# Optimization experiments

Measured on AMD Instinct MI355X. Metric: run time of the kernel, lower is better.

## Reference

```python
import jax, jax.numpy as jnp
import numpy as np

N = 100000   # nodes
H = 96       # hidden_dim
A = 32       # attn_dim
De = 16      # edge_embeddings_dim
E = 500000   # edges per edge type
NEG_SLOPE = 0.01  # torch F.leaky_relu default


def setup_inputs() -> dict:
    key = jax.random.key(0)
    ks = jax.random.split(key, 24)
    nrm = lambda k, shape, s=1.0: jax.random.normal(k, shape, dtype=jnp.float32) * s
    idx = lambda k: jax.random.randint(k, (E,), 0, N, dtype=jnp.int32)
    Din = 2 * H + De
    return {
        'h': nrm(ks[0], (N, H)),
        'src0': idx(ks[1]), 'dst0': idx(ks[2]),
        'src1': idx(ks[3]), 'dst1': idx(ks[4]),
        'src2': idx(ks[5]), 'dst2': idx(ks[6]),
        'Wm0': nrm(ks[7], (Din, H), Din ** -0.5), 'bm0': jnp.zeros((H,), jnp.float32), 'ef0': nrm(ks[8], (De,)),
        'Wm1': nrm(ks[9], (Din, H), Din ** -0.5), 'bm1': jnp.zeros((H,), jnp.float32), 'ef1': nrm(ks[10], (De,)),
        'Wm2': nrm(ks[11], (Din, H), Din ** -0.5), 'bm2': jnp.zeros((H,), jnp.float32), 'ef2': nrm(ks[12], (De,)),
        'Wn0': nrm(ks[13], (H, A), H ** -0.5), 'Wa0': nrm(ks[14], (2 * A, 1), (2 * A) ** -0.5),
        'Wn1': nrm(ks[15], (H, A), H ** -0.5), 'Wa1': nrm(ks[16], (2 * A, 1), (2 * A) ** -0.5),
        'Wu': nrm(ks[17], (4 * H, H), (4 * H) ** -0.5), 'bu': jnp.zeros((H,), jnp.float32),
    }


def _leaky(x):
    return jnp.where(x > 0, x, NEG_SLOPE * x)


def _edge_msg(h, src, dst, Wm, bm, ef):
    # cat(src_h, dst_h, edge_feature) -> Linear  (dropout p=0, eval mode)
    x = jnp.concatenate([h[src], h[dst], jnp.broadcast_to(ef, (src.shape[0], ef.shape[0]))], axis=-1)
    return x @ Wm + bm  # [E, H]


def _mean_agg(m, dst):
    # fn.mean('m','msg'): per-destination mean over incoming edges
    s = jax.ops.segment_sum(m, dst, num_segments=N)
    c = jax.ops.segment_sum(jnp.ones((m.shape[0],), m.dtype), dst, num_segments=N)
    return s / jnp.maximum(c, 1.0)[:, None]


def _attn_agg(scores, m, dst):
    # per-destination softmax over mailbox (variable-size), then weighted sum
    smax = jax.ops.segment_max(scores, dst, num_segments=N)
    ex = jnp.exp(scores - smax[dst])
    den = jax.ops.segment_sum(ex, dst, num_segments=N)
    num = jax.ops.segment_sum(ex[:, None] * m, dst, num_segments=N)
    return num / jnp.maximum(den, 1e-9)[:, None]


def reference(h, src0, dst0, src1, dst1, src2, dst2,
              Wm0, bm0, ef0, Wm1, bm1, ef1, Wm2, bm2, ef2,
              Wn0, Wa0, Wn1, Wa1, Wu, bu):
    # edge type 0: intra_diff (attention), type 1: inter_diff (attention), type 2: intra_lt (mean)
    m0 = _edge_msg(h, src0, dst0, Wm0, bm0, ef0)
    m1 = _edge_msg(h, src1, dst1, Wm1, bm1, ef1)
    m2 = _edge_msg(h, src2, dst2, Wm2, bm2, ef2)

    z0 = h @ Wn0  # [N, A]
    s0 = _leaky(jnp.concatenate([z0[src0], z0[dst0]], axis=-1) @ Wa0)[:, 0]  # [E]
    z1 = h @ Wn1
    s1 = _leaky(jnp.concatenate([z1[src1], z1[dst1]], axis=-1) @ Wa1)[:, 0]

    msg0 = _attn_agg(s0, m0, dst0)   # [N, H]
    msg1 = _attn_agg(s1, m1, dst1)
    msg2 = _mean_agg(m2, dst2)

    # cross_reducer='stack' then concat over edge-type dim -> [N, 3H]
    mcat = jnp.concatenate([msg0, msg1, msg2], axis=-1)
    # cell node update: Linear(cat(h, m)) + ReLU
    return jax.nn.relu(jnp.concatenate([h, mcat], axis=-1) @ Wu + bu)
```

## Files before the change

kernel.cpp:

```cpp
#include <hip/hip_runtime.h>
#include <hip/hip_bf16.h>
#include <cstdint>

#define NN 100000
#define HH 96
#define AD 32
#define DE 16
#define EE 500000
#define NEG 0.01f

#define GSH 10
#define GSZ 1024
#define KB 98
#define CH 4096
#define BPT 123

typedef __bf16 bf16x8 __attribute__((ext_vector_type(8)));
typedef float  f32x4  __attribute__((ext_vector_type(4)));

__device__ __forceinline__ unsigned short f2b(float x) {
    union { float f; unsigned int u; } v; v.f = x;
    unsigned int r = v.u + 0x7fffu + ((v.u >> 16) & 1u);
    return (unsigned short)(r >> 16);
}
__device__ __forceinline__ float b2f(unsigned short h) {
    union { unsigned int u; float f; } v; v.u = ((unsigned int)h) << 16;
    return v.f;
}

__global__ void prep_kernel(const float* Wm0, const float* bm0, const float* ef0,
                            const float* Wm1, const float* bm1, const float* ef1,
                            const float* Wm2, const float* bm2, const float* ef2,
                            const float* Wn0, const float* Wa0,
                            const float* Wn1, const float* Wa1,
                            const float* Wu,
                            float* cvec, float* wvec,
                            unsigned short* BfN, unsigned short* BfU) {
    const float* Wm[3] = {Wm0, Wm1, Wm2};
    const float* bm[3] = {bm0, bm1, bm2};
    const float* ef[3] = {ef0, ef1, ef2};
    const int total = 288 + 384 + 55296 + 36864;
    for (int i = blockIdx.x * blockDim.x + threadIdx.x; i < total;
         i += gridDim.x * blockDim.x) {
        if (i < 288) {
            int t = i / 96, j = i % 96;
            float s = bm[t][j];
            for (int k = 0; k < DE; ++k) s += ef[t][k] * Wm[t][(2 * HH + k) * HH + j];
            cvec[i] = s;
        } else if (i < 288 + 384) {
            int ii = i - 288;
            int kind = ii / 96, k = ii % 96;
            const float* Wn = (kind < 2) ? Wn0 : Wn1;
            const float* Wa = (kind < 2) ? Wa0 : Wa1;
            int off = (kind & 1) ? AD : 0;
            float s = 0.f;
            for (int a = 0; a < AD; ++a) s += Wn[k * AD + a] * Wa[off + a];
            wvec[ii] = s;
        } else if (i < 288 + 384 + 55296) {
            int ii = i - 672;
            int sec = ii / 9216; int rem = ii % 9216;
            int ksc = rem / 512; int lj = rem % 512;
            int ks = ksc / 6, c = ksc % 6;
            int lane = lj / 8, jj = lj % 8;
            int quad = lane / 16, m = lane % 16;
            int k = ks * 32 + quad * 8 + jj;
            int n = c * 16 + m;
            int mt = (sec < 3) ? sec : sec - 3;
            int rowoff = (sec < 3) ? 0 : HH;
            BfN[ii] = f2b(Wm[mt][(rowoff + k) * HH + n]);
        } else {
            int ii = i - (672 + 55296);
            int ksc = ii / 512; int lj = ii % 512;
            int ks = ksc / 6, c = ksc % 6;
            int lane = lj / 8, jj = lj % 8;
            int quad = lane / 16, m = lane % 16;
            int k = ks * 32 + quad * 8 + jj;
            int n = c * 16 + m;
            BfU[ii] = f2b(Wu[k * HH + n]);
        }
    }
}

__global__ void cast_uv_kernel(const float* __restrict__ h, const float* __restrict__ wvec,
                               unsigned short* __restrict__ hb, float* __restrict__ uv) {
    int lane = threadIdx.x & 31;
    int node = (blockIdx.x * blockDim.x + threadIdx.x) >> 5;
    if (node >= NN) return;
    float h0 = h[node * HH + lane];
    float h1 = h[node * HH + 32 + lane];
    float h2 = h[node * HH + 64 + lane];
    hb[node * HH + lane] = f2b(h0);
    hb[node * HH + 32 + lane] = f2b(h1);
    hb[node * HH + 64 + lane] = f2b(h2);
    float acc[4];
#pragma unroll
    for (int q = 0; q < 4; ++q)
        acc[q] = h0 * wvec[q * 96 + lane] + h1 * wvec[q * 96 + 32 + lane] +
                 h2 * wvec[q * 96 + 64 + lane];
#pragma unroll
    for (int d = 16; d >= 1; d >>= 1)
#pragma unroll
        for (int q = 0; q < 4; ++q) acc[q] += __shfl_down(acc[q], d, 32);
    if (lane == 0) {
#pragma unroll
        for (int q = 0; q < 4; ++q) uv[q * NN + node] = acc[q];
    }
}

__global__ void zero_kernel(float4* __restrict__ p, int n4) {
    for (int i = blockIdx.x * blockDim.x + threadIdx.x; i < n4;
         i += gridDim.x * blockDim.x)
        p[i] = make_float4(0.f, 0.f, 0.f, 0.f);
}

__global__ void bucket_hist(const int* __restrict__ d0, const int* __restrict__ d1,
                            const int* __restrict__ d2, int* __restrict__ bCnt) {
    __shared__ int hist[3 * KB];
    int t = threadIdx.x;
    for (int j = t; j < 3 * KB; j += 256) hist[j] = 0;
    __syncthreads();
    const int total = 3 * EE;
    for (int i = blockIdx.x * blockDim.x + t; i < total; i += gridDim.x * blockDim.x) {
        int ty = i / EE, e = i - ty * EE;
        const int* d = (ty == 0) ? d0 : (ty == 1) ? d1 : d2;
        atomicAdd(&hist[ty * KB + (d[e] >> GSH)], 1);
    }
    __syncthreads();
    for (int j = t; j < 3 * KB; j += 256)
        if (hist[j]) atomicAdd(&bCnt[j], hist[j]);
}

__global__ void bucket_scan(const int* __restrict__ bCnt, int* __restrict__ bBase,
                            int* __restrict__ gCursor, int* __restrict__ rs) {
    __shared__ int hist[3 * KB];
    int t = threadIdx.x;
    if (t < 3 * KB) hist[t] = bCnt[t];
    __syncthreads();
    if (t < 3) {
        int run = 0;
        for (int b = 0; b < KB; ++b) {
            bBase[t * (KB + 1) + b] = run;
            gCursor[t * KB + b] = run;
            run += hist[t * KB + b];
        }
        bBase[t * (KB + 1) + KB] = run;
        rs[(size_t)t * (NN + 1) + NN] = run;
    }
}

__global__ __launch_bounds__(256) void bucket_scatter(
    const int* __restrict__ s0, const int* __restrict__ d0,
    const int* __restrict__ s1, const int* __restrict__ d1,
    const int* __restrict__ s2, const int* __restrict__ d2,
    int* __restrict__ gCursor, unsigned int* __restrict__ binned) {
    __shared__ unsigned int recs[CH];
    __shared__ unsigned short rnk[CH];
    __shared__ unsigned char bkt[CH];
    __shared__ int cnt[KB];
    __shared__ int gpos[KB];
    int t = threadIdx.x;
    int type = blockIdx.x / BPT;
    int chunk = (blockIdx.x % BPT) * CH;
    const int* src = (type == 0) ? s0 : (type == 1) ? s1 : s2;
    const int* dst = (type == 0) ? d0 : (type == 1) ? d1 : d2;
    if (t < KB) cnt[t] = 0;
    __syncthreads();
#pragma unroll
    for (int k = 0; k < CH / 256; ++k) {
        int idx = k * 256 + t;
        int e = chunk + idx;
        if (e < EE) {
            int s = src[e], d = dst[e];
            int b = d >> GSH;
            recs[idx] = ((unsigned int)s << GSH) | (unsigned int)(d & (GSZ - 1));
            bkt[idx] = (unsigned char)b;
            rnk[idx] = (unsigned short)atomicAdd(&cnt[b], 1);
        } else {
            bkt[idx] = 0xFF;
        }
    }
    __syncthreads();
    if (t < KB) {
        int c = cnt[t];
        gpos[t] = (c > 0) ? atomicAdd(&gCursor[type * KB + t], c) : 0;
    }
    __syncthreads();
    unsigned int* bout = binned + (size_t)type * EE;
#pragma unroll
    for (int k = 0; k < CH / 256; ++k) {
        int idx = k * 256 + t;
        unsigned char b = bkt[idx];
        if (b != 0xFF) bout[gpos[b] + rnk[idx]] = recs[idx];
    }
}

__global__ __launch_bounds__(256) void bucket_sort(
    const unsigned int* __restrict__ binned, const int* __restrict__ bBase,
    int* __restrict__ rs, int* __restrict__ sorted) {
    __shared__ int cnt[GSZ];
    __shared__ int tsum[256];
    int t = threadIdx.x;
    int type = blockIdx.x / KB;
    int b = blockIdx.x % KB;
    int nodeBase = b * GSZ;
    int eb = bBase[type * (KB + 1) + b];
    int en = bBase[type * (KB + 1) + b + 1];
    int n = en - eb;
    const unsigned int* bin = binned + (size_t)type * EE + eb;
#pragma unroll
    for (int k = 0; k < GSZ / 256; ++k) cnt[k * 256 + t] = 0;
    __syncthreads();
    for (int i = t; i < n; i += 256) atomicAdd(&cnt[bin[i] & (GSZ - 1)], 1);
    __syncthreads();
    int v[4], s = 0;
#pragma unroll
    for (int k = 0; k < 4; ++k) { v[k] = cnt[t * 4 + k]; s += v[k]; }
    tsum[t] = s;
    __syncthreads();
    for (int off = 1; off < 256; off <<= 1) {
        int add = (t >= off) ? tsum[t - off] : 0;
        __syncthreads();
        tsum[t] += add;
        __syncthreads();
    }
    int run = tsum[t] - s;
    int offk[4];
#pragma unroll
    for (int k = 0; k < 4; ++k) { offk[k] = run; run += v[k]; }
    int* rsrow = rs + (size_t)type * (NN + 1) + nodeBase;
#pragma unroll
    for (int k = 0; k < 4; ++k) {
        int node = t * 4 + k;
        if (nodeBase + node < NN) rsrow[node] = eb + offk[k];
    }
    __syncthreads();
#pragma unroll
    for (int k = 0; k < 4; ++k) cnt[t * 4 + k] = offk[k];
    __syncthreads();
    int* so = sorted + (size_t)type * EE + eb;
    for (int i = t; i < n; i += 256) {
        unsigned int r = bin[i];
        int dl = r & (GSZ - 1);
        int p = atomicAdd(&cnt[dl], 1);
        so[p] = (int)(r >> GSH);
    }
}

__global__ void aggregate_kernel(const int* __restrict__ rsAll, const int* __restrict__ sortedAll,
                                 const float* __restrict__ uv,
                                 const unsigned short* __restrict__ hb,
                                 unsigned short* __restrict__ hagg,
                                 float* __restrict__ den) {
    const size_t NH = (size_t)NN * HH;
    int lane = threadIdx.x & 31;
    int node = (blockIdx.x * blockDim.x + threadIdx.x) >> 5;
    if (node >= NN) return;
    int t = blockIdx.y;
    int is_attn = (t < 2);
    const int* rs = rsAll + (size_t)t * (NN + 1);
    const int* sorted = sortedAll + (size_t)t * EE;
    const float* u = uv + 2 * t * NN;

    int beg = rs[node], end = rs[node + 1];
    float a0 = 0.f, a1 = 0.f, a2 = 0.f, dn = 0.f;
    float vd = is_attn ? uv[(2 * t + 1) * NN + node] : 0.f;
    for (int base = beg; base < end; base += 32) {
        int batch = end - base;
        if (batch > 32) batch = 32;
        int li = lane < batch ? lane : batch - 1;
        int myS = sorted[base + li];
#pragma unroll 1
        for (int j = 0; j < batch; j += 8) {
            int rem = batch - j;
            int sI[8];
            float wv[8];
#pragma unroll
            for (int k = 0; k < 8; ++k) sI[k] = __shfl(myS, (k < rem ? j + k : j), 32);
            if (is_attn) {
#pragma unroll
                for (int k = 0; k < 8; ++k) {
                    float c = u[sI[k]] + vd;
                    c = c > 0.f ? c : NEG * c;
                    wv[k] = __expf(c);
                }
            } else {
#pragma unroll
                for (int k = 0; k < 8; ++k) wv[k] = 1.f;
            }
#pragma unroll
            for (int k = 0; k < 8; ++k) if (k >= rem) wv[k] = 0.f;
            float x0[8], x1[8], x2[8];
#pragma unroll
            for (int k = 0; k < 8; ++k) {
                const unsigned short* pr = hb + (size_t)sI[k] * HH;
                x0[k] = b2f(pr[lane]);
                x1[k] = b2f(pr[lane + 32]);
                x2[k] = b2f(pr[lane + 64]);
            }
#pragma unroll
            for (int k = 0; k < 8; ++k) {
                dn += wv[k];
                a0 += wv[k] * x0[k];
                a1 += wv[k] * x1[k];
                a2 += wv[k] * x2[k];
            }
        }
    }
    float r0 = 0.f, r1 = 0.f, r2 = 0.f;
    if (dn > 0.f) {
        float inv = 1.f / dn;
        r0 = a0 * inv; r1 = a1 * inv; r2 = a2 * inv;
    }
    unsigned short* mr = hagg + (size_t)t * NH + (size_t)node * HH;
    mr[lane] = f2b(r0);
    mr[lane + 32] = f2b(r1);
    mr[lane + 64] = f2b(r2);
    if (lane == 0) den[(size_t)t * NN + node] = dn;
}

__global__ __launch_bounds__(256) void msg_gemm_kernel(const unsigned short* __restrict__ hagg,
                                                       const unsigned short* __restrict__ hb,
                                                       const unsigned short* __restrict__ BfN,
                                                       const float* __restrict__ den,
                                                       const float* __restrict__ cvec,
                                                       unsigned short* __restrict__ msgb) {
    const size_t NH = (size_t)NN * HH;
    int wave = threadIdx.x >> 6;
    int lane = threadIdx.x & 63;
    int quad = lane >> 4, m = lane & 15;
    int blk = blockIdx.x * 4 + wave;
    if (blk >= NN / 16) return;
    int t = blockIdx.y;
    int r0 = blk * 16;
    const unsigned short* ha = hagg + (size_t)t * NH;
    f32x4 acc[6] = {};
#pragma unroll
    for (int ks = 0; ks < 6; ++ks) {
        const unsigned short* ap =
            (ks < 3) ? ha + (size_t)(r0 + m) * HH + ks * 32 + quad * 8
                     : hb + (size_t)(r0 + m) * HH + (ks - 3) * 32 + quad * 8;
        int sec = (ks < 3) ? t : t + 3;
        int kk = (ks < 3) ? ks : ks - 3;
        bf16x8 af = *(const bf16x8*)ap;
#pragma unroll
        for (int c = 0; c < 6; ++c) {
            bf16x8 bfv = *(const bf16x8*)(BfN + (((sec * 3 + kk) * 6 + c) << 9) + lane * 8);
            acc[c] = __builtin_amdgcn_mfma_f32_16x16x32_bf16(af, bfv, acc[c], 0, 0, 0);
        }
    }
    float dn[4];
#pragma unroll
    for (int r = 0; r < 4; ++r) dn[r] = den[(size_t)t * NN + r0 + quad * 4 + r];
#pragma unroll
    for (int c = 0; c < 6; ++c) {
        float cv = cvec[t * 96 + c * 16 + m];
#pragma unroll
        for (int r = 0; r < 4; ++r) {
            int row = r0 + quad * 4 + r;
            float val = (dn[r] > 0.f) ? (acc[c][r] + cv) : 0.f;
            msgb[(size_t)row * 288 + t * 96 + c * 16 + m] = f2b(val);
        }
    }
}

__global__ __launch_bounds__(256) void update_gemm_kernel(const unsigned short* __restrict__ hb,
                                                          const unsigned short* __restrict__ msgb,
                                                          const unsigned short* __restrict__ BfU,
                                                          const float* __restrict__ bu,
                                                          float* __restrict__ out) {
    int wave = threadIdx.x >> 6;
    int lane = threadIdx.x & 63;
    int quad = lane >> 4, m = lane & 15;
    int blk = blockIdx.x * 4 + wave;
    if (blk >= NN / 16) return;
    int r0 = blk * 16;
    f32x4 acc[6] = {};
#pragma unroll
    for (int ks = 0; ks < 12; ++ks) {
        const unsigned short* ap =
            (ks < 3) ? hb + (size_t)(r0 + m) * HH + ks * 32 + quad * 8
                     : msgb + (size_t)(r0 + m) * 288 + (ks - 3) * 32 + quad * 8;
        bf16x8 af = *(const bf16x8*)ap;
#pragma unroll
        for (int c = 0; c < 6; ++c) {
            bf16x8 bfv = *(const bf16x8*)(BfU + ((ks * 6 + c) << 9) + lane * 8);
            acc[c] = __builtin_amdgcn_mfma_f32_16x16x32_bf16(af, bfv, acc[c], 0, 0, 0);
        }
    }
#pragma unroll
    for (int c = 0; c < 6; ++c) {
        float b = bu[c * 16 + m];
#pragma unroll
        for (int r = 0; r < 4; ++r) {
            int row = r0 + quad * 4 + r;
            float v2 = acc[c][r] + b;
            out[(size_t)row * HH + c * 16 + m] = v2 > 0.f ? v2 : 0.f;
        }
    }
}

extern "C" void kernel_launch(void* const* d_in, const int* in_sizes, int n_in,
                              void* d_out, int out_size, void* d_ws, size_t ws_size,
                              hipStream_t stream) {
    (void)in_sizes; (void)n_in; (void)out_size;
    const float* h   = (const float*)d_in[0];
    const int* srcs[3] = {(const int*)d_in[1], (const int*)d_in[3], (const int*)d_in[5]};
    const int* dsts[3] = {(const int*)d_in[2], (const int*)d_in[4], (const int*)d_in[6]};
    const float* Wm0 = (const float*)d_in[7];
    const float* bm0 = (const float*)d_in[8];
    const float* ef0 = (const float*)d_in[9];
    const float* Wm1 = (const float*)d_in[10];
    const float* bm1 = (const float*)d_in[11];
    const float* ef1 = (const float*)d_in[12];
    const float* Wm2 = (const float*)d_in[13];
    const float* bm2 = (const float*)d_in[14];
    const float* ef2 = (const float*)d_in[15];
    const float* Wn0 = (const float*)d_in[16];
    const float* Wa0 = (const float*)d_in[17];
    const float* Wn1 = (const float*)d_in[18];
    const float* Wa1 = (const float*)d_in[19];
    const float* Wu  = (const float*)d_in[20];
    const float* bu  = (const float*)d_in[21];
    float* out = (float*)d_out;

    const size_t NEED = 150591104;
    if (ws_size < NEED) return;
    char* w = (char*)d_ws;
    unsigned short* msgb    = (unsigned short*)(w + 0);
    unsigned short* hb      = (unsigned short*)(w + 57600000);
    unsigned short* hagg    = (unsigned short*)(w + 76800000);
    float*          den     = (float*)(w + 134400000);
    float*          uv      = (float*)(w + 135600000);
    float*          cvec    = (float*)(w + 137200000);
    float*          wvec    = (float*)(w + 137201280);
    unsigned short* BfN     = (unsigned short*)(w + 137202816);
    unsigned short* BfU     = (unsigned short*)(w + 137313408);
    int*            bBase   = (int*)(w + 137387136);
    int*            gCursor = (int*)(w + 137388416);
    int*            bCnt    = (int*)(w + 137389696);
    int*            rs      = (int*)(w + 137390976);
    int*            sorted  = (int*)(w + 138591104);
    unsigned int*   binned  = (unsigned int*)(w + 144591104);

    prep_kernel<<<128, 256, 0, stream>>>(Wm0, bm0, ef0, Wm1, bm1, ef1, Wm2, bm2, ef2,
                                         Wn0, Wa0, Wn1, Wa1, Wu, cvec, wvec, BfN, BfU);
    cast_uv_kernel<<<12500, 256, 0, stream>>>(h, wvec, hb, uv);

    zero_kernel<<<1, 256, 0, stream>>>((float4*)bCnt, 80);
    bucket_hist<<<512, 256, 0, stream>>>(dsts[0], dsts[1], dsts[2], bCnt);
    bucket_scan<<<1, 384, 0, stream>>>(bCnt, bBase, gCursor, rs);
    bucket_scatter<<<3 * BPT, 256, 0, stream>>>(srcs[0], dsts[0], srcs[1], dsts[1],
                                                srcs[2], dsts[2], gCursor, binned);
    bucket_sort<<<3 * KB, 256, 0, stream>>>(binned, bBase, rs, sorted);

    aggregate_kernel<<<dim3(12500, 3), 256, 0, stream>>>(rs, sorted, uv, hb, hagg, den);
    msg_gemm_kernel<<<dim3(1563, 3), 256, 0, stream>>>(hagg, hb, BfN, den, cvec, msgb);
    update_gemm_kernel<<<1563, 256, 0, stream>>>(hb, msgb, BfU, bu, out);
}
```

Measured before the change: 330.9 us.

## Precompute edge attention weights during histogram and pack them into sorted edge records

The exp(leaky(u_src+v_dst)) attention weight is now computed per edge inside the histogram pass and written to a temporary array. The scatter and sort stages carry it in 64-bit records alongside a precomputed byte offset into the bf16 node table. The aggregate kernel therefore streams (weight, offset) pairs with a simple unrolled-by-4 loop, replacing the shuffle-based gather and the per-edge exp. This removes the uv gathers and the shuffles from the hot aggregation loop. In exchange it doubles the bytes moved through scatter and sort, adds a weight array write and read, and grows the workspace. Reads past the end of the last segment are covered by zeroing padding records.

```diff
diff --git a/kernel.cpp b/kernel.cpp
--- a/kernel.cpp
+++ b/kernel.cpp
@@ -17,6 +17,7 @@
 
 typedef __bf16 bf16x8 __attribute__((ext_vector_type(8)));
 typedef float  f32x4  __attribute__((ext_vector_type(4)));
+typedef unsigned long long ull;
 
 __device__ __forceinline__ unsigned short f2b(float x) {
     union { float f; unsigned int u; } v; v.f = x;
@@ -113,8 +114,11 @@
         p[i] = make_float4(0.f, 0.f, 0.f, 0.f);
 }
 
-__global__ void bucket_hist(const int* __restrict__ d0, const int* __restrict__ d1,
-                            const int* __restrict__ d2, int* __restrict__ bCnt) {
+__global__ void bucket_hist(const int* __restrict__ s0, const int* __restrict__ d0,
+                            const int* __restrict__ s1, const int* __restrict__ d1,
+                            const int* __restrict__ s2, const int* __restrict__ d2,
+                            const float* __restrict__ uv,
+                            int* __restrict__ bCnt, float* __restrict__ wtmp) {
     __shared__ int hist[3 * KB];
     int t = threadIdx.x;
     for (int j = t; j < 3 * KB; j += 256) hist[j] = 0;
@@ -122,8 +126,16 @@
     const int total = 3 * EE;
     for (int i = blockIdx.x * blockDim.x + t; i < total; i += gridDim.x * blockDim.x) {
         int ty = i / EE, e = i - ty * EE;
-        const int* d = (ty == 0) ? d0 : (ty == 1) ? d1 : d2;
-        atomicAdd(&hist[ty * KB + (d[e] >> GSH)], 1);
+        const int* dp = (ty == 0) ? d0 : (ty == 1) ? d1 : d2;
+        int d = dp[e];
+        atomicAdd(&hist[ty * KB + (d >> GSH)], 1);
+        if (ty < 2) {
+            const int* sp = (ty == 0) ? s0 : s1;
+            int s = sp[e];
+            float c = uv[2 * ty * NN + s] + uv[(2 * ty + 1) * NN + d];
+            c = c > 0.f ? c : NEG * c;
+            wtmp[(size_t)ty * EE + e] = __expf(c);
+        }
     }
     __syncthreads();
     for (int j = t; j < 3 * KB; j += 256)
@@ -131,10 +143,12 @@
 }
 
 __global__ void bucket_scan(const int* __restrict__ bCnt, int* __restrict__ bBase,
-                            int* __restrict__ gCursor, int* __restrict__ rs) {
+                            int* __restrict__ gCursor, int* __restrict__ rs,
+                            ull* __restrict__ wrec) {
     __shared__ int hist[3 * KB];
     int t = threadIdx.x;
     if (t < 3 * KB) hist[t] = bCnt[t];
+    if (t < 8) wrec[(size_t)3 * EE + t] = 0ull;
     __syncthreads();
     if (t < 3) {
         int run = 0;
@@ -152,8 +166,9 @@
     const int* __restrict__ s0, const int* __restrict__ d0,
     const int* __restrict__ s1, const int* __restrict__ d1,
     const int* __restrict__ s2, const int* __restrict__ d2,
-    int* __restrict__ gCursor, unsigned int* __restrict__ binned) {
-    __shared__ unsigned int recs[CH];
+    const float* __restrict__ wtmp,
+    int* __restrict__ gCursor, ull* __restrict__ binned) {
+    __shared__ ull recs[CH];
     __shared__ unsigned short rnk[CH];
     __shared__ unsigned char bkt[CH];
     __shared__ int cnt[KB];
@@ -172,7 +187,9 @@
         if (e < EE) {
             int s = src[e], d = dst[e];
             int b = d >> GSH;
-            recs[idx] = ((unsigned int)s << GSH) | (unsigned int)(d & (GSZ - 1));
+            float w = (type < 2) ? wtmp[(size_t)type * EE + e] : 1.0f;
+            recs[idx] = ((ull)__float_as_uint(w) << 32) |
+                        ((unsigned int)s << GSH) | (unsigned int)(d & (GSZ - 1));
             bkt[idx] = (unsigned char)b;
             rnk[idx] = (unsigned short)atomicAdd(&cnt[b], 1);
         } else {
@@ -185,7 +202,7 @@
         gpos[t] = (c > 0) ? atomicAdd(&gCursor[type * KB + t], c) : 0;
     }
     __syncthreads();
-    unsigned int* bout = binned + (size_t)type * EE;
+    ull* bout = binned + (size_t)type * EE;
 #pragma unroll
     for (int k = 0; k < CH / 256; ++k) {
         int idx = k * 256 + t;
@@ -195,8 +212,8 @@
 }
 
 __global__ __launch_bounds__(256) void bucket_sort(
-    const unsigned int* __restrict__ binned, const int* __restrict__ bBase,
-    int* __restrict__ rs, int* __restrict__ sorted) {
+    const ull* __restrict__ binned, const int* __restrict__ bBase,
+    int* __restrict__ rs, ull* __restrict__ wrec) {
     __shared__ int cnt[GSZ];
     __shared__ int tsum[256];
     int t = threadIdx.x;
@@ -206,11 +223,12 @@
     int eb = bBase[type * (KB + 1) + b];
     int en = bBase[type * (KB + 1) + b + 1];
     int n = en - eb;
-    const unsigned int* bin = binned + (size_t)type * EE + eb;
+    const ull* bin = binned + (size_t)type * EE + eb;
+    const unsigned int* binlo = (const unsigned int*)bin;
 #pragma unroll
     for (int k = 0; k < GSZ / 256; ++k) cnt[k * 256 + t] = 0;
     __syncthreads();
-    for (int i = t; i < n; i += 256) atomicAdd(&cnt[bin[i] & (GSZ - 1)], 1);
+    for (int i = t; i < n; i += 256) atomicAdd(&cnt[binlo[2 * i] & (GSZ - 1)], 1);
     __syncthreads();
     int v[4], s = 0;
 #pragma unroll
@@ -237,17 +255,19 @@
 #pragma unroll
     for (int k = 0; k < 4; ++k) cnt[t * 4 + k] = offk[k];
     __syncthreads();
-    int* so = sorted + (size_t)type * EE + eb;
+    ull* wo = wrec + (size_t)type * EE + eb;
     for (int i = t; i < n; i += 256) {
-        unsigned int r = bin[i];
-        int dl = r & (GSZ - 1);
+        ull r = bin[i];
+        unsigned int lo = (unsigned int)r;
+        int dl = lo & (GSZ - 1);
         int p = atomicAdd(&cnt[dl], 1);
-        so[p] = (int)(r >> GSH);
-    }
-}
-
-__global__ void aggregate_kernel(const int* __restrict__ rsAll, const int* __restrict__ sortedAll,
-                                 const float* __restrict__ uv,
+        unsigned int off = (lo >> GSH) * 192u;
+        wo[p] = (r & 0xFFFFFFFF00000000ull) | (ull)off;
+    }
+}
+
+__global__ void aggregate_kernel(const int* __restrict__ rsAll,
+                                 const ull* __restrict__ wrec,
                                  const unsigned short* __restrict__ hb,
                                  unsigned short* __restrict__ hagg,
                                  float* __restrict__ den) {
@@ -256,65 +276,37 @@
     int node = (blockIdx.x * blockDim.x + threadIdx.x) >> 5;
     if (node >= NN) return;
     int t = blockIdx.y;
-    int is_attn = (t < 2);
     const int* rs = rsAll + (size_t)t * (NN + 1);
-    const int* sorted = sortedAll + (size_t)t * EE;
-    const float* u = uv + 2 * t * NN;
-
+    const ull* wr = wrec + (size_t)t * EE;
     int beg = rs[node], end = rs[node + 1];
     float a0 = 0.f, a1 = 0.f, a2 = 0.f, dn = 0.f;
-    float vd = is_attn ? uv[(2 * t + 1) * NN + node] : 0.f;
-    for (int base = beg; base < end; base += 32) {
-        int batch = end - base;
-        if (batch > 32) batch = 32;
-        int li = lane < batch ? lane : batch - 1;
-        int myS = sorted[base + li];
-#pragma unroll 1
-        for (int j = 0; j < batch; j += 8) {
-            int rem = batch - j;
-            int sI[8];
-            float wv[8];
-#pragma unroll
-            for (int k = 0; k < 8; ++k) sI[k] = __shfl(myS, (k < rem ? j + k : j), 32);
-            if (is_attn) {
-#pragma unroll
-                for (int k = 0; k < 8; ++k) {
-                    float c = u[sI[k]] + vd;
-                    c = c > 0.f ? c : NEG * c;
-                    wv[k] = __expf(c);
-                }
-            } else {
-#pragma unroll
-                for (int k = 0; k < 8; ++k) wv[k] = 1.f;
-            }
-#pragma unroll
-            for (int k = 0; k < 8; ++k) if (k >= rem) wv[k] = 0.f;
-            float x0[8], x1[8], x2[8];
-#pragma unroll
-            for (int k = 0; k < 8; ++k) {
-                const unsigned short* pr = hb + (size_t)sI[k] * HH;
-                x0[k] = b2f(pr[lane]);
-                x1[k] = b2f(pr[lane + 32]);
-                x2[k] = b2f(pr[lane + 64]);
-            }
-#pragma unroll
-            for (int k = 0; k < 8; ++k) {
-                dn += wv[k];
-                a0 += wv[k] * x0[k];
-                a1 += wv[k] * x1[k];
-                a2 += wv[k] * x2[k];
-            }
-        }
-    }
-    float r0 = 0.f, r1 = 0.f, r2 = 0.f;
-    if (dn > 0.f) {
-        float inv = 1.f / dn;
-        r0 = a0 * inv; r1 = a1 * inv; r2 = a2 * inv;
-    }
-    unsigned short* mr = hagg + (size_t)t * NH + (size_t)node * HH;
-    mr[lane] = f2b(r0);
-    mr[lane + 32] = f2b(r1);
-    mr[lane + 64] = f2b(r2);
+    const char* b0 = (const char*)hb + 4 * lane;
+    const char* b1 = (const char*)hb + 128 + 2 * lane;
+#define EDGE(rec, cond)                                                        \
+    {                                                                          \
+        float w = (cond) ? __uint_as_float((unsigned int)((rec) >> 32)) : 0.f; \
+        unsigned int off = (unsigned int)(rec);                                \
+        unsigned int dv = *(const unsigned int*)(b0 + off);                    \
+        unsigned int sv = *(const unsigned short*)(b1 + off);                  \
+        a0 += w * __uint_as_float(dv << 16);                                   \
+        a1 += w * __uint_as_float(dv & 0xFFFF0000u);                           \
+        a2 += w * __uint_as_float(sv << 16);                                   \
+        dn += w;                                                               \
+    }
+    for (int j = beg; j < end; j += 4) {
+        ull r0 = wr[j], r1 = wr[j + 1], r2 = wr[j + 2], r3 = wr[j + 3];
+        EDGE(r0, true);
+        EDGE(r1, j + 1 < end);
+        EDGE(r2, j + 2 < end);
+        EDGE(r3, j + 3 < end);
+    }
+#undef EDGE
+    float inv = (dn > 0.f) ? 1.f / dn : 0.f;
+    float q0 = a0 * inv, q1 = a1 * inv, q2 = a2 * inv;
+    char* mr = (char*)(hagg + (size_t)t * NH + (size_t)node * HH);
+    *(unsigned int*)(mr + 4 * lane) =
+        (unsigned int)f2b(q0) | ((unsigned int)f2b(q1) << 16);
+    *(unsigned short*)(mr + 128 + 2 * lane) = f2b(q2);
     if (lane == 0) den[(size_t)t * NN + node] = dn;
 }
 
@@ -423,7 +415,7 @@
     const float* bu  = (const float*)d_in[21];
     float* out = (float*)d_out;
 
-    const size_t NEED = 150591104;
+    const size_t NEED = 166591232;
     if (ws_size < NEED) return;
     char* w = (char*)d_ws;
     unsigned short* msgb    = (unsigned short*)(w + 0);
@@ -439,21 +431,23 @@
     int*            gCursor = (int*)(w + 137388416);
     int*            bCnt    = (int*)(w + 137389696);
     int*            rs      = (int*)(w + 137390976);
-    int*            sorted  = (int*)(w + 138591104);
-    unsigned int*   binned  = (unsigned int*)(w + 144591104);
+    ull*            wrec    = (ull*)(w + 138591104);
+    ull*            binned  = (ull*)(w + 150591232);
+    float*          wtmp    = (float*)(w + 162591232);
 
     prep_kernel<<<128, 256, 0, stream>>>(Wm0, bm0, ef0, Wm1, bm1, ef1, Wm2, bm2, ef2,
                                          Wn0, Wa0, Wn1, Wa1, Wu, cvec, wvec, BfN, BfU);
     cast_uv_kernel<<<12500, 256, 0, stream>>>(h, wvec, hb, uv);
 
     zero_kernel<<<1, 256, 0, stream>>>((float4*)bCnt, 80);
-    bucket_hist<<<512, 256, 0, stream>>>(dsts[0], dsts[1], dsts[2], bCnt);
-    bucket_scan<<<1, 384, 0, stream>>>(bCnt, bBase, gCursor, rs);
+    bucket_hist<<<512, 256, 0, stream>>>(srcs[0], dsts[0], srcs[1], dsts[1],
+                                         srcs[2], dsts[2], uv, bCnt, wtmp);
+    bucket_scan<<<1, 384, 0, stream>>>(bCnt, bBase, gCursor, rs, wrec);
     bucket_scatter<<<3 * BPT, 256, 0, stream>>>(srcs[0], dsts[0], srcs[1], dsts[1],
-                                                srcs[2], dsts[2], gCursor, binned);
-    bucket_sort<<<3 * KB, 256, 0, stream>>>(binned, bBase, rs, sorted);
-
-    aggregate_kernel<<<dim3(12500, 3), 256, 0, stream>>>(rs, sorted, uv, hb, hagg, den);
+                                                srcs[2], dsts[2], wtmp, gCursor, binned);
+    bucket_sort<<<3 * KB, 256, 0, stream>>>(binned, bBase, rs, wrec);
+
+    aggregate_kernel<<<dim3(12500, 3), 256, 0, stream>>>(rs, wrec, hb, hagg, den);
     msg_gemm_kernel<<<dim3(1563, 3), 256, 0, stream>>>(hagg, hb, BfN, den, cvec, msgb);
     update_gemm_kernel<<<1563, 256, 0, stream>>>(hb, msgb, BfU, bu, out);
 }
```

New measurement: 331.1 us. No clear change (+0.0%).
